# Kernel tuning notes

Measured on AMD Instinct MI355X. Metric: run time of the kernel, lower is better.

Reference implementation:

```python
import jax, jax.numpy as jnp
import numpy as np

DELTA_V = 0.5
DELTA_D = 1.5
ALPHA = 1.0
BETA = 1.0
GAMMA = 0.001
K = 33  # label ids 0..32; 0 = background (ignored)
EPS = 1e-12


def setup_inputs() -> dict:
    key = jax.random.key(0)
    k1, k2 = jax.random.split(key)
    B, N, E = 8, 65536, 32
    embeddings = jax.random.normal(k1, (B, N, E), dtype=jnp.float32)
    labels = jax.random.randint(k2, (B, N), 0, K)
    return {"embeddings": embeddings, "labels": labels}


def reference(embeddings, labels):
    B, N, E = embeddings.shape
    dt = embeddings.dtype
    seg = (labels + jnp.arange(B)[:, None] * K).reshape(-1)  # (B*N,)

    # segment mean -> per-instance centers (B, K, E)
    sums = jax.ops.segment_sum(embeddings.reshape(B * N, E), seg, num_segments=B * K).reshape(B, K, E)
    counts = jax.ops.segment_sum(jnp.ones((B * N,), dtype=dt), seg, num_segments=B * K).reshape(B, K)
    centers = sums / jnp.maximum(counts, 1.0)[..., None]

    present = counts > 0
    present = present.at[:, 0].set(False)  # drop background label 0
    presf = present.astype(dt)
    n_inst = presf.sum(axis=1)  # (B,)

    # ---- variance term: per-point hinge distance to own center, segment-mean ----
    c_per_point = centers[jnp.arange(B)[:, None], labels]  # (B, N, E) gather
    d2 = ((embeddings - c_per_point) ** 2).sum(-1)
    dist = jnp.sqrt(jnp.maximum(d2, EPS))
    hinge = jnp.where(labels > 0, jnp.maximum(dist - DELTA_V, 0.0), 0.0)
    per_inst_sum = jax.ops.segment_sum(hinge.reshape(-1), seg, num_segments=B * K).reshape(B, K)
    per_inst_mean = per_inst_sum / jnp.maximum(counts, 1.0)
    variance_term = (per_inst_mean * presf).sum(1) / jnp.maximum(n_inst, 1.0)

    # ---- distance term: pairwise hinge between present instance centers ----
    diff2 = ((centers[:, :, None, :] - centers[:, None, :, :]) ** 2).sum(-1)  # (B,K,K)
    upper = jnp.triu(jnp.ones((K, K), dtype=bool), 1)[None]
    pair_valid = present[:, :, None] & present[:, None, :] & upper
    cd = jnp.sqrt(jnp.maximum(jnp.where(pair_valid, diff2, 1.0), EPS))
    pair_hinge = jnp.maximum(2.0 * DELTA_D - cd, 0.0) * pair_valid.astype(dt)
    n_pairs = n_inst * (n_inst - 1.0) * 0.5
    distance_term = pair_hinge.sum((1, 2)) / jnp.maximum(n_pairs, 1.0)

    # ---- regularization: mean L2 norm of present centers ----
    c_norm = jnp.sqrt(jnp.maximum((centers ** 2).sum(-1), EPS))
    reg_term = (c_norm * presf).sum(1) / jnp.maximum(n_inst, 1.0)

    per_batch = ALPHA * variance_term + BETA * distance_term + GAMMA * reg_term
    per_batch = jnp.where(n_inst > 0, per_batch, 0.0)
    return per_batch.sum() / B
```

## Files before the change

kernel.cpp:

```cpp
#include <hip/hip_runtime.h>
#include <math.h>

#define KC 33
#define ED 32
#define KE (KC * ED)
#define BPB 128
#define TP 128
#define NSLOT 8


__global__ void k_zero(float* __restrict__ ws, int n, float* __restrict__ out) {
    int i = blockIdx.x * blockDim.x + threadIdx.x;
    if (i < n) ws[i] = 0.f;
    if (i == 0) out[0] = 0.f;
}

__global__ __launch_bounds__(256) void k_accum(const float* __restrict__ emb,
                                               const int* __restrict__ lab,
                                               float* __restrict__ sums,
                                               float* __restrict__ counts,
                                               int N) {
    __shared__ __align__(16) float s_tile[TP * ED];
    __shared__ float s_priv[NSLOT * KE];
    __shared__ float s_cntp[NSLOT * KC];
    __shared__ int   s_lab[TP];
    int t = threadIdx.x;
    for (int i = t; i < NSLOT * KE; i += 256) s_priv[i] = 0.f;
    for (int i = t; i < NSLOT * KC; i += 256) s_cntp[i] = 0.f;

    int b     = blockIdx.x / BPB;
    int blk   = blockIdx.x % BPB;
    int chunk = N / BPB;
    int e     = t & 31;
    int slot  = t >> 5;
    size_t pbase = (size_t)b * N + (size_t)blk * chunk;
    __syncthreads();

    for (int tb = 0; tb < chunk / TP; tb++) {
        size_t tstart = pbase + (size_t)tb * TP;
        const float4* g4 = (const float4*)(emb + tstart * ED);
        float4* s4 = (float4*)s_tile;
#pragma unroll
        for (int r = 0; r < (TP * ED / 4) / 256; r++)
            s4[t + r * 256] = g4[t + r * 256];
        if (t < TP) s_lab[t] = lab[tstart + t];
        __syncthreads();

#pragma unroll 4
        for (int step = 0; step < TP / NSLOT; step++) {
            int pt = step * NSLOT + slot;
            float x = s_tile[pt * ED + e];
            int k = s_lab[pt];
            s_priv[slot * KE + k * ED + e] += x;
            if (e == 0) s_cntp[slot * KC + k] += 1.f;
        }
        __syncthreads();
    }

    for (int i = t; i < KE; i += 256) {
        float v = 0.f;
#pragma unroll
        for (int s = 0; s < NSLOT; s++) v += s_priv[s * KE + i];
        atomicAdd(&sums[(size_t)b * KE + i], v);
    }
    if (t < KC) {
        float v = 0.f;
#pragma unroll
        for (int s = 0; s < NSLOT; s++) v += s_cntp[s * KC + t];
        atomicAdd(&counts[b * KC + t], v);
    }
}

__global__ void k_centers(const float* __restrict__ sums,
                          const float* __restrict__ counts,
                          float* __restrict__ ctr, float* __restrict__ inv, int B) {
    int i = blockIdx.x * blockDim.x + threadIdx.x;
    int tot1 = B * KE;
    if (i < tot1) {
        ctr[i] = sums[i] / fmaxf(counts[i / ED], 1.0f);
    } else if (i < tot1 + B * KC) {
        int j = i - tot1;
        int k = j % KC;
        inv[j] = (k > 0) ? 1.0f / fmaxf(counts[j], 1.0f) : 0.f;
    }
}

__global__ __launch_bounds__(256) void k_hinge(const float* __restrict__ emb,
                                               const int* __restrict__ lab,
                                               const float* __restrict__ ctr,
                                               const float* __restrict__ inv,
                                               float* __restrict__ var, int N) {
    __shared__ __align__(16) float s_tile[TP * ED];
    __shared__ float s_ctr[KE];
    __shared__ float s_inv[KC];
    __shared__ int   s_lab[TP];
    __shared__ float s_red[4];
    int t    = threadIdx.x;
    int b    = blockIdx.x / BPB;
    int blk  = blockIdx.x % BPB;
    int chunk = N / BPB;
    int e    = t & 31;
    int slot = t >> 5;
    size_t pbase = (size_t)b * N + (size_t)blk * chunk;

    for (int i = t; i < KE; i += 256) s_ctr[i] = ctr[(size_t)b * KE + i];
    if (t < KC) s_inv[t] = inv[b * KC + t];
    float hs = 0.f;

    for (int tb = 0; tb < chunk / TP; tb++) {
        size_t tstart = pbase + (size_t)tb * TP;
        const float4* g4 = (const float4*)(emb + tstart * ED);
        float4* s4 = (float4*)s_tile;
#pragma unroll
        for (int r = 0; r < (TP * ED / 4) / 256; r++)
            s4[t + r * 256] = g4[t + r * 256];
        if (t < TP) s_lab[t] = lab[tstart + t];
        __syncthreads();

#pragma unroll 4
        for (int step = 0; step < TP / NSLOT; step++) {
            int pt = step * NSLOT + slot;
            float x = s_tile[pt * ED + e];
            int k = s_lab[pt];
            float d = x - s_ctr[k * ED + e];
            float d2 = d * d;
            d2 += __shfl_xor(d2, 1);
            d2 += __shfl_xor(d2, 2);
            d2 += __shfl_xor(d2, 4);
            d2 += __shfl_xor(d2, 8);
            d2 += __shfl_xor(d2, 16);
            float dist = sqrtf(fmaxf(d2, 1e-12f));
            hs += fmaxf(dist - 0.5f, 0.f) * s_inv[k];
        }
        __syncthreads();
    }

    hs += __shfl_xor(hs, 1);
    hs += __shfl_xor(hs, 2);
    hs += __shfl_xor(hs, 4);
    hs += __shfl_xor(hs, 8);
    hs += __shfl_xor(hs, 16);
    hs += __shfl_xor(hs, 32);
    if ((t & 63) == 0) s_red[t >> 6] = hs;
    __syncthreads();
    if (t == 0) {
        float v = s_red[0] + s_red[1] + s_red[2] + s_red[3];
        atomicAdd(&var[b], v * (1.0f / 32.0f));
    }
}

__global__ __launch_bounds__(256) void k_final(const float* __restrict__ counts,
                                               const float* __restrict__ var,
                                               const float* __restrict__ ctr,
                                               float* __restrict__ out, int B) {
    __shared__ float s_ctr[KE];
    __shared__ float s_reg[KC];
    __shared__ int   s_prs[KC];
    __shared__ float s_red[256];
    int b = blockIdx.x;
    int t = threadIdx.x;

    for (int i = t; i < KE; i += 256) s_ctr[i] = ctr[(size_t)b * KE + i];
    if (t < KC) {
        float cnt = counts[b * KC + t];
        s_prs[t] = (t > 0 && cnt > 0.f) ? 1 : 0;
    }
    __syncthreads();
    if (t < KC) {
        float n2 = 0.f;
        for (int e2 = 0; e2 < ED; e2++) { float c = s_ctr[t * ED + e2]; n2 += c * c; }
        s_reg[t] = s_prs[t] ? sqrtf(fmaxf(n2, 1e-12f)) : 0.f;
    }
    __syncthreads();

    float psum = 0.f;
    for (int q = t; q < KC * KC; q += 256) {
        int i = q / KC, j = q % KC;
        if (i < j && s_prs[i] && s_prs[j]) {
            float d2 = 0.f;
            for (int e2 = 0; e2 < ED; e2++) {
                float d = s_ctr[i * ED + e2] - s_ctr[j * ED + e2];
                d2 += d * d;
            }
            float cd = sqrtf(fmaxf(d2, 1e-12f));
            psum += fmaxf(3.0f - cd, 0.f);
        }
    }
    s_red[t] = psum;
    __syncthreads();
    for (int s = 128; s > 0; s >>= 1) {
        if (t < s) s_red[t] += s_red[t + s];
        __syncthreads();
    }

    if (t == 0) {
        float reg = 0.f; int n = 0;
        for (int k = 0; k < KC; k++) { reg += s_reg[k]; n += s_prs[k]; }
        float nf = (float)n;
        float variance_term = var[b] / fmaxf(nf, 1.f);
        float npairs = nf * (nf - 1.f) * 0.5f;
        float distance_term = s_red[0] / fmaxf(npairs, 1.f);
        float reg_term = reg / fmaxf(nf, 1.f);
        float pb = variance_term + distance_term + 0.001f * reg_term;
        if (n == 0) pb = 0.f;
        atomicAdd(out, pb / (float)B);
    }
}

extern "C" void kernel_launch(void* const* d_in, const int* in_sizes, int n_in,
                              void* d_out, int out_size, void* d_ws, size_t ws_size,
                              hipStream_t stream) {
    const float* emb = (const float*)d_in[0];
    const int*   lab = (const int*)d_in[1];
    float* out = (float*)d_out;

    const int B = 8;
    const int N = in_sizes[1] / B;

    float* sums   = (float*)d_ws;
    float* counts = sums + (size_t)B * KE;
    float* var    = counts + (size_t)B * KC;
    float* ctr    = var + B;
    float* inv    = ctr + (size_t)B * KE;

    int zn = B * KE + B * KC + B;
    k_zero<<<(zn + 255) / 256, 256, 0, stream>>>(sums, zn, out);
    k_accum<<<B * BPB, 256, 0, stream>>>(emb, lab, sums, counts, N);
    int cn = B * KE + B * KC;
    k_centers<<<(cn + 255) / 256, 256, 0, stream>>>(sums, counts, ctr, inv, B);
    k_hinge<<<B * BPB, 256, 0, stream>>>(emb, lab, ctr, inv, var, N);
    k_final<<<B, 256, 0, stream>>>(counts, var, ctr, out, B);
}
```

Measured before the change: 153.7 us.

## Restructure pipeline: separate label histogram, register prefetch, per-thread hinge, fold centers kernel

Label counting moves into a separate histogram kernel, and the centers kernel is removed: hinge and final now compute centers from sums and counts in shared memory. Accumulate and hinge prefetch the next tile into registers while the current tile is processed, and use a padded shared-memory layout to avoid bank conflicts. Hinge now computes each point's full 32-dim distance in one thread, replacing the warp shuffle reduction. The accumulate grid is halved and the hinge tile doubled, which cuts launches and shuffles but raises register pressure.

```diff
diff --git a/kernel.cpp b/kernel.cpp
--- a/kernel.cpp
+++ b/kernel.cpp
@@ -4,9 +4,13 @@
 #define KC 33
 #define ED 32
 #define KE (KC * ED)
-#define BPB 128
-#define TP 128
+#define PAD 33
+
+#define BPB_A 64
+#define TPA 128
 #define NSLOT 8
+#define BPB_H 128
+#define TPH 256
 
 
 __global__ void k_zero(float* __restrict__ ws, int n, float* __restrict__ out) {
@@ -15,44 +19,79 @@
     if (i == 0) out[0] = 0.f;
 }
 
+__global__ __launch_bounds__(256) void k_hist(const int* __restrict__ lab,
+                                              float* __restrict__ counts, int N) {
+    __shared__ float h[4 * KC];
+    int t = threadIdx.x;
+    int w = t >> 6;
+    if (t < 4 * KC) h[t] = 0.f;
+    __syncthreads();
+    int b   = blockIdx.x >> 5;
+    int blk = blockIdx.x & 31;
+    const int4* l4 = (const int4*)(lab + (size_t)b * N + (size_t)blk * 2048);
+    int4 a = l4[t];
+    int4 c = l4[t + 256];
+    float* hw = &h[w * KC];
+    atomicAdd(&hw[a.x], 1.f); atomicAdd(&hw[a.y], 1.f);
+    atomicAdd(&hw[a.z], 1.f); atomicAdd(&hw[a.w], 1.f);
+    atomicAdd(&hw[c.x], 1.f); atomicAdd(&hw[c.y], 1.f);
+    atomicAdd(&hw[c.z], 1.f); atomicAdd(&hw[c.w], 1.f);
+    __syncthreads();
+    if (t < KC)
+        atomicAdd(&counts[b * KC + t], h[t] + h[KC + t] + h[2 * KC + t] + h[3 * KC + t]);
+}
+
 __global__ __launch_bounds__(256) void k_accum(const float* __restrict__ emb,
                                                const int* __restrict__ lab,
-                                               float* __restrict__ sums,
-                                               float* __restrict__ counts,
-                                               int N) {
-    __shared__ __align__(16) float s_tile[TP * ED];
+                                               float* __restrict__ sums, int N) {
+    __shared__ float s_tile[TPA * PAD];
     __shared__ float s_priv[NSLOT * KE];
-    __shared__ float s_cntp[NSLOT * KC];
-    __shared__ int   s_lab[TP];
+    __shared__ int   s_lab[TPA];
     int t = threadIdx.x;
     for (int i = t; i < NSLOT * KE; i += 256) s_priv[i] = 0.f;
-    for (int i = t; i < NSLOT * KC; i += 256) s_cntp[i] = 0.f;
-
-    int b     = blockIdx.x / BPB;
-    int blk   = blockIdx.x % BPB;
-    int chunk = N / BPB;
+
+    int b     = blockIdx.x / BPB_A;
+    int blk   = blockIdx.x % BPB_A;
+    int chunk = N / BPB_A;
     int e     = t & 31;
     int slot  = t >> 5;
     size_t pbase = (size_t)b * N + (size_t)blk * chunk;
-    __syncthreads();
-
-    for (int tb = 0; tb < chunk / TP; tb++) {
-        size_t tstart = pbase + (size_t)tb * TP;
-        const float4* g4 = (const float4*)(emb + tstart * ED);
-        float4* s4 = (float4*)s_tile;
+    const int NT = chunk / TPA;
+
+    const float4* g4 = (const float4*)(emb + pbase * ED);
+    float4 r0 = g4[t], r1 = g4[t + 256], r2 = g4[t + 512], r3 = g4[t + 768];
+    int rl = 0;
+    if (t < TPA) rl = lab[pbase + t];
+    __syncthreads();
+
+    for (int tb = 0; tb < NT; tb++) {
+        {
+            int f, p, m;
+            f = t;        p = f >> 3; m = (f & 7) * 4;
+            { float* d = &s_tile[PAD * p + m]; d[0]=r0.x; d[1]=r0.y; d[2]=r0.z; d[3]=r0.w; }
+            f = t + 256;  p = f >> 3; m = (f & 7) * 4;
+            { float* d = &s_tile[PAD * p + m]; d[0]=r1.x; d[1]=r1.y; d[2]=r1.z; d[3]=r1.w; }
+            f = t + 512;  p = f >> 3; m = (f & 7) * 4;
+            { float* d = &s_tile[PAD * p + m]; d[0]=r2.x; d[1]=r2.y; d[2]=r2.z; d[3]=r2.w; }
+            f = t + 768;  p = f >> 3; m = (f & 7) * 4;
+            { float* d = &s_tile[PAD * p + m]; d[0]=r3.x; d[1]=r3.y; d[2]=r3.z; d[3]=r3.w; }
+        }
+        if (t < TPA) s_lab[t] = rl;
+        __syncthreads();
+
+        if (tb + 1 < NT) {
+            const float4* gn = (const float4*)(emb + (pbase + (size_t)(tb + 1) * TPA) * ED);
+            r0 = gn[t]; r1 = gn[t + 256]; r2 = gn[t + 512]; r3 = gn[t + 768];
+            if (t < TPA) rl = lab[pbase + (size_t)(tb + 1) * TPA + t];
+        }
+
+        float* priv = &s_priv[slot * KE];
 #pragma unroll
-        for (int r = 0; r < (TP * ED / 4) / 256; r++)
-            s4[t + r * 256] = g4[t + r * 256];
-        if (t < TP) s_lab[t] = lab[tstart + t];
-        __syncthreads();
-
-#pragma unroll 4
-        for (int step = 0; step < TP / NSLOT; step++) {
-            int pt = step * NSLOT + slot;
-            float x = s_tile[pt * ED + e];
-            int k = s_lab[pt];
-            s_priv[slot * KE + k * ED + e] += x;
-            if (e == 0) s_cntp[slot * KC + k] += 1.f;
+        for (int st = 0; st < TPA / NSLOT; st++) {
+            int pt = st * NSLOT + slot;
+            float x = s_tile[pt * PAD + e];
+            int   k = s_lab[pt];
+            priv[k * ED + e] += x;
         }
         __syncthreads();
     }
@@ -63,108 +102,116 @@
         for (int s = 0; s < NSLOT; s++) v += s_priv[s * KE + i];
         atomicAdd(&sums[(size_t)b * KE + i], v);
     }
-    if (t < KC) {
-        float v = 0.f;
-#pragma unroll
-        for (int s = 0; s < NSLOT; s++) v += s_cntp[s * KC + t];
-        atomicAdd(&counts[b * KC + t], v);
-    }
-}
-
-__global__ void k_centers(const float* __restrict__ sums,
-                          const float* __restrict__ counts,
-                          float* __restrict__ ctr, float* __restrict__ inv, int B) {
-    int i = blockIdx.x * blockDim.x + threadIdx.x;
-    int tot1 = B * KE;
-    if (i < tot1) {
-        ctr[i] = sums[i] / fmaxf(counts[i / ED], 1.0f);
-    } else if (i < tot1 + B * KC) {
-        int j = i - tot1;
-        int k = j % KC;
-        inv[j] = (k > 0) ? 1.0f / fmaxf(counts[j], 1.0f) : 0.f;
-    }
 }
 
 __global__ __launch_bounds__(256) void k_hinge(const float* __restrict__ emb,
                                                const int* __restrict__ lab,
-                                               const float* __restrict__ ctr,
-                                               const float* __restrict__ inv,
+                                               const float* __restrict__ sums,
+                                               const float* __restrict__ counts,
                                                float* __restrict__ var, int N) {
-    __shared__ __align__(16) float s_tile[TP * ED];
-    __shared__ float s_ctr[KE];
+    __shared__ float s_tile[TPH * PAD];
+    __shared__ float s_ctr[KC * PAD];
+    __shared__ float s_cnt[KC];
     __shared__ float s_inv[KC];
-    __shared__ int   s_lab[TP];
+    __shared__ int   s_lab[TPH];
     __shared__ float s_red[4];
-    int t    = threadIdx.x;
-    int b    = blockIdx.x / BPB;
-    int blk  = blockIdx.x % BPB;
-    int chunk = N / BPB;
-    int e    = t & 31;
-    int slot = t >> 5;
+    int t     = threadIdx.x;
+    int b     = blockIdx.x / BPB_H;
+    int blk   = blockIdx.x % BPB_H;
+    int chunk = N / BPB_H;
     size_t pbase = (size_t)b * N + (size_t)blk * chunk;
-
-    for (int i = t; i < KE; i += 256) s_ctr[i] = ctr[(size_t)b * KE + i];
-    if (t < KC) s_inv[t] = inv[b * KC + t];
+    const int NT = chunk / TPH;
+
+    const float4* g4 = (const float4*)(emb + pbase * ED);
+    float4 r0 = g4[t],        r1 = g4[t + 256],  r2 = g4[t + 512],  r3 = g4[t + 768];
+    float4 r4 = g4[t + 1024], r5 = g4[t + 1280], r6 = g4[t + 1536], r7 = g4[t + 1792];
+    int rl = lab[pbase + t];
+
+    if (t < KC) {
+        float c = counts[b * KC + t];
+        s_cnt[t] = fmaxf(c, 1.f);
+        s_inv[t] = (t > 0 && c > 0.f) ? 1.f / fmaxf(c, 1.f) : 0.f;
+    }
+    __syncthreads();
+    for (int i = t; i < KE; i += 256) {
+        int k = i >> 5, e = i & 31;
+        s_ctr[k * PAD + e] = sums[(size_t)b * KE + i] / s_cnt[k];
+    }
+
     float hs = 0.f;
-
-    for (int tb = 0; tb < chunk / TP; tb++) {
-        size_t tstart = pbase + (size_t)tb * TP;
-        const float4* g4 = (const float4*)(emb + tstart * ED);
-        float4* s4 = (float4*)s_tile;
+    for (int tb = 0; tb < NT; tb++) {
+        {
+            int f, p, m;
+            f = t;         p = f >> 3; m = (f & 7) * 4;
+            { float* d = &s_tile[PAD * p + m]; d[0]=r0.x; d[1]=r0.y; d[2]=r0.z; d[3]=r0.w; }
+            f = t + 256;   p = f >> 3; m = (f & 7) * 4;
+            { float* d = &s_tile[PAD * p + m]; d[0]=r1.x; d[1]=r1.y; d[2]=r1.z; d[3]=r1.w; }
+            f = t + 512;   p = f >> 3; m = (f & 7) * 4;
+            { float* d = &s_tile[PAD * p + m]; d[0]=r2.x; d[1]=r2.y; d[2]=r2.z; d[3]=r2.w; }
+            f = t + 768;   p = f >> 3; m = (f & 7) * 4;
+            { float* d = &s_tile[PAD * p + m]; d[0]=r3.x; d[1]=r3.y; d[2]=r3.z; d[3]=r3.w; }
+            f = t + 1024;  p = f >> 3; m = (f & 7) * 4;
+            { float* d = &s_tile[PAD * p + m]; d[0]=r4.x; d[1]=r4.y; d[2]=r4.z; d[3]=r4.w; }
+            f = t + 1280;  p = f >> 3; m = (f & 7) * 4;
+            { float* d = &s_tile[PAD * p + m]; d[0]=r5.x; d[1]=r5.y; d[2]=r5.z; d[3]=r5.w; }
+            f = t + 1536;  p = f >> 3; m = (f & 7) * 4;
+            { float* d = &s_tile[PAD * p + m]; d[0]=r6.x; d[1]=r6.y; d[2]=r6.z; d[3]=r6.w; }
+            f = t + 1792;  p = f >> 3; m = (f & 7) * 4;
+            { float* d = &s_tile[PAD * p + m]; d[0]=r7.x; d[1]=r7.y; d[2]=r7.z; d[3]=r7.w; }
+        }
+        s_lab[t] = rl;
+        __syncthreads();
+
+        if (tb + 1 < NT) {
+            const float4* gn = (const float4*)(emb + (pbase + (size_t)(tb + 1) * TPH) * ED);
+            r0 = gn[t];        r1 = gn[t + 256];  r2 = gn[t + 512];  r3 = gn[t + 768];
+            r4 = gn[t + 1024]; r5 = gn[t + 1280]; r6 = gn[t + 1536]; r7 = gn[t + 1792];
+            rl = lab[pbase + (size_t)(tb + 1) * TPH + t];
+        }
+
+        int   k  = s_lab[t];
+        float iv = s_inv[k];
+        const float* xr = &s_tile[t * PAD];
+        const float* cr = &s_ctr[k * PAD];
+        float d2 = 0.f;
 #pragma unroll
-        for (int r = 0; r < (TP * ED / 4) / 256; r++)
-            s4[t + r * 256] = g4[t + r * 256];
-        if (t < TP) s_lab[t] = lab[tstart + t];
-        __syncthreads();
-
-#pragma unroll 4
-        for (int step = 0; step < TP / NSLOT; step++) {
-            int pt = step * NSLOT + slot;
-            float x = s_tile[pt * ED + e];
-            int k = s_lab[pt];
-            float d = x - s_ctr[k * ED + e];
-            float d2 = d * d;
-            d2 += __shfl_xor(d2, 1);
-            d2 += __shfl_xor(d2, 2);
-            d2 += __shfl_xor(d2, 4);
-            d2 += __shfl_xor(d2, 8);
-            d2 += __shfl_xor(d2, 16);
-            float dist = sqrtf(fmaxf(d2, 1e-12f));
-            hs += fmaxf(dist - 0.5f, 0.f) * s_inv[k];
-        }
-        __syncthreads();
-    }
-
-    hs += __shfl_xor(hs, 1);
-    hs += __shfl_xor(hs, 2);
-    hs += __shfl_xor(hs, 4);
-    hs += __shfl_xor(hs, 8);
-    hs += __shfl_xor(hs, 16);
-    hs += __shfl_xor(hs, 32);
+        for (int j = 0; j < ED; j++) {
+            float d = xr[j] - cr[j];
+            d2 = fmaf(d, d, d2);
+        }
+        float dist = sqrtf(fmaxf(d2, 1e-12f));
+        hs += fmaxf(dist - 0.5f, 0.f) * iv;
+        __syncthreads();
+    }
+
+    hs += __shfl_xor(hs, 1);  hs += __shfl_xor(hs, 2);  hs += __shfl_xor(hs, 4);
+    hs += __shfl_xor(hs, 8);  hs += __shfl_xor(hs, 16); hs += __shfl_xor(hs, 32);
     if ((t & 63) == 0) s_red[t >> 6] = hs;
     __syncthreads();
-    if (t == 0) {
-        float v = s_red[0] + s_red[1] + s_red[2] + s_red[3];
-        atomicAdd(&var[b], v * (1.0f / 32.0f));
-    }
-}
-
-__global__ __launch_bounds__(256) void k_final(const float* __restrict__ counts,
+    if (t == 0)
+        atomicAdd(&var[b], s_red[0] + s_red[1] + s_red[2] + s_red[3]);
+}
+
+__global__ __launch_bounds__(256) void k_final(const float* __restrict__ sums,
+                                               const float* __restrict__ counts,
                                                const float* __restrict__ var,
-                                               const float* __restrict__ ctr,
                                                float* __restrict__ out, int B) {
     __shared__ float s_ctr[KE];
+    __shared__ float s_cnt[KC];
     __shared__ float s_reg[KC];
     __shared__ int   s_prs[KC];
     __shared__ float s_red[256];
     int b = blockIdx.x;
     int t = threadIdx.x;
 
-    for (int i = t; i < KE; i += 256) s_ctr[i] = ctr[(size_t)b * KE + i];
     if (t < KC) {
-        float cnt = counts[b * KC + t];
-        s_prs[t] = (t > 0 && cnt > 0.f) ? 1 : 0;
-    }
+        float c = counts[b * KC + t];
+        s_cnt[t] = fmaxf(c, 1.f);
+        s_prs[t] = (t > 0 && c > 0.f) ? 1 : 0;
+    }
+    __syncthreads();
+    for (int i = t; i < KE; i += 256)
+        s_ctr[i] = sums[(size_t)b * KE + i] / s_cnt[i >> 5];
     __syncthreads();
     if (t < KC) {
         float n2 = 0.f;
@@ -220,14 +267,11 @@
     float* sums   = (float*)d_ws;
     float* counts = sums + (size_t)B * KE;
     float* var    = counts + (size_t)B * KC;
-    float* ctr    = var + B;
-    float* inv    = ctr + (size_t)B * KE;
 
     int zn = B * KE + B * KC + B;
     k_zero<<<(zn + 255) / 256, 256, 0, stream>>>(sums, zn, out);
-    k_accum<<<B * BPB, 256, 0, stream>>>(emb, lab, sums, counts, N);
-    int cn = B * KE + B * KC;
-    k_centers<<<(cn + 255) / 256, 256, 0, stream>>>(sums, counts, ctr, inv, B);
-    k_hinge<<<B * BPB, 256, 0, stream>>>(emb, lab, ctr, inv, var, N);
-    k_final<<<B, 256, 0, stream>>>(counts, var, ctr, out, B);
-}
+    k_hist<<<B * 32, 256, 0, stream>>>(lab, counts, N);
+    k_accum<<<B * BPB_A, 256, 0, stream>>>(emb, lab, sums, N);
+    k_hinge<<<B * BPB_H, 256, 0, stream>>>(emb, lab, sums, counts, var, N);
+    k_final<<<B, 256, 0, stream>>>(sums, counts, var, out, B);
+}
```

Result: faster. 134.1 us (-12.7%).
